# Optimization experiments

Hardware: AMD Instinct MI355X
Metric: run time of the kernel (lower is better)

Reference implementation:

```python
import jax, jax.numpy as jnp
import numpy as np

N, F_IN, HID, C, H = 4096, 1024, 64, 40, 8
ALPHA = 0.2  # LeakyReLU negative slope
NEG_INF = -9e15

def setup_inputs() -> dict:
    key = jax.random.key(0)
    ks = jax.random.split(key, 8)
    x = jax.random.normal(ks[0], (N, F_IN), jnp.float32)
    adj = jax.random.randint(ks[1], (N, N), 0, 2, jnp.int32)  # dense 0/1 adjacency
    W = jax.random.normal(ks[2], (H, F_IN, HID), jnp.float32) / np.sqrt(F_IN).astype(np.float32)
    a_src = jax.random.normal(ks[3], (H, HID), jnp.float32) * 0.1
    a_dst = jax.random.normal(ks[4], (H, HID), jnp.float32) * 0.1
    W_out = jax.random.normal(ks[5], (H * HID, C), jnp.float32) / np.sqrt(H * HID).astype(np.float32)
    ao_src = jax.random.normal(ks[6], (C,), jnp.float32) * 0.1
    ao_dst = jax.random.normal(ks[7], (C,), jnp.float32) * 0.1
    return dict(x=x, adj=adj, W=W, a_src=a_src, a_dst=a_dst,
                W_out=W_out, ao_src=ao_src, ao_dst=ao_dst)

def _masked_attention(src, dst, mask):
    # src: [..., N] scores for row node i; dst: [..., N] scores for col node j
    e = jax.nn.leaky_relu(src[..., :, None] + dst[..., None, :], ALPHA)  # [..., N, N]
    e = jnp.where(mask, e, NEG_INF)
    return jax.nn.softmax(e, axis=-1)

def reference(x, adj, W, a_src, a_dst, W_out, ao_src, ao_dst):
    mask = adj > 0  # [N, N]
    # multi-head GAT layer (concat=True)
    Wh = jnp.einsum('nf,hfo->hno', x, W)            # [H, N, HID]
    src = jnp.einsum('hno,ho->hn', Wh, a_src)       # [H, N]
    dst = jnp.einsum('hno,ho->hn', Wh, a_dst)       # [H, N]
    att = _masked_attention(src, dst, mask[None])   # [H, N, N]
    h = jnp.einsum('hij,hjo->hio', att, Wh)         # [H, N, HID]
    h = jax.nn.elu(h)                               # concat=True -> elu inside layer
    h = jnp.transpose(h, (1, 0, 2)).reshape(N, H * HID)  # concat heads -> [N, H*HID]
    # output GAT layer (concat=False -> no elu inside)
    Wh2 = h @ W_out                                 # [N, C]
    att2 = _masked_attention(Wh2 @ ao_src, Wh2 @ ao_dst, mask)  # [N, N]
    out = att2 @ Wh2                                # [N, C]
    # model-level: elu then log_softmax over classes
    return jax.nn.log_softmax(jax.nn.elu(out), axis=1)
```

## Files before the change

### kernel.cpp

```cpp
#include <hip/hip_runtime.h>

#define NN 4096
#define F_IN 1024
#define NHEAD 8
#define HID 64
#define NCLS 40
#define LOG2E 1.44269504f

typedef float f32x4 __attribute__((ext_vector_type(4)));
typedef float f32x2 __attribute__((ext_vector_type(2)));
typedef short s16x8 __attribute__((ext_vector_type(8)));

#define SWZ(r,c) (((r)*64) + ((c) ^ (((r)&7)<<3)))

__device__ __forceinline__ unsigned short f2bf(float f){
  unsigned u = __float_as_uint(f);
  return (unsigned short)((u + 0x7fffu + ((u >> 16) & 1u)) >> 16);
}
__device__ __forceinline__ unsigned cvtpk(float lo, float hi){
  unsigned r; asm("v_cvt_pk_bf16_f32 %0, %1, %2" : "=v"(r) : "v"(lo), "v"(hi)); return r;
}
__device__ __forceinline__ f32x2 pkmul(f32x2 a, f32x2 b){
  f32x2 r; asm("v_pk_mul_f32 %0, %1, %2" : "=v"(r) : "v"(a), "v"(b)); return r;
}

__global__ __launch_bounds__(256) void pack_adj_k(const int* __restrict__ adj, unsigned* __restrict__ bmT){
  int gid = blockIdx.x*256 + threadIdx.x;
  int lane = threadIdx.x & 63;
  unsigned long long m = __ballot(adj[gid] > 0);
  int w = gid >> 5, i = w >> 7, jw = w & 127;
  if (lane == 0)       bmT[(size_t)jw*NN + i] = (unsigned)m;
  else if (lane == 32) bmT[(size_t)jw*NN + i] = (unsigned)(m >> 32);
}

__global__ __launch_bounds__(256) void cast_W_k(const float* __restrict__ W, unsigned short* __restrict__ WbT){
  __shared__ float T[64][65];
  const int h = blockIdx.y, k0 = blockIdx.x*64, t = threadIdx.x;
  for (int idx = t; idx < 1024; idx += 256){
    int k = idx >> 4, c4 = idx & 15;
    *(float4*)&T[k][c4*4] = *(const float4*)&W[((size_t)h*F_IN + k0 + k)*HID + c4*4];
  }
  __syncthreads();
  for (int idx = t; idx < 512; idx += 256){
    int o = idx >> 3, ch = idx & 7;
    s16x8 v;
    #pragma unroll
    for (int e = 0; e < 8; ++e) v[e] = (short)f2bf(T[ch*8 + e][o]);
    *(s16x8*)&WbT[((size_t)h*HID + o)*F_IN + k0 + ch*8] = v;
  }
}

__global__ __launch_bounds__(256) void cast_Wo_k(const float* __restrict__ Wout, unsigned short* __restrict__ WoT){
  int idx = blockIdx.x*256 + threadIdx.x;
  int cc = idx >> 9, k = idx & 511;
  WoT[idx] = (cc < NCLS) ? f2bf(Wout[(size_t)k*NCLS + cc]) : (unsigned short)0;
}

__global__ __launch_bounds__(256) void gemm1_k(const float* __restrict__ x,
    const unsigned short* __restrict__ WbT, unsigned short* __restrict__ WhT,
    const float* __restrict__ a_src, const float* __restrict__ a_dst,
    float* __restrict__ srcv, float* __restrict__ dstv){
  __shared__ unsigned short xS[64*64];
  __shared__ unsigned short wS[64*64];
  const int t = threadIdx.x, l = t & 63, wv = t >> 6, g = l >> 4, c = l & 15;
  const int h = blockIdx.y, n0 = blockIdx.x * 64;
  f32x4 acc[4] = {};
  for (int k0 = 0; k0 < F_IN; k0 += 64){
    __syncthreads();
    #pragma unroll
    for (int p = 0; p < 4; ++p){
      int idx = t + p*256, row = idx >> 4, c4 = idx & 15;
      float4 v = *(const float4*)&x[(size_t)(n0+row)*F_IN + k0 + c4*4];
      *(uint2*)&xS[SWZ(row, c4*4)] = make_uint2(cvtpk(v.x, v.y), cvtpk(v.z, v.w));
    }
    #pragma unroll
    for (int p = 0; p < 2; ++p){
      int idx = t + p*256, o = idx >> 3, ch = idx & 7;
      *(s16x8*)&wS[SWZ(o, ch*8)] = *(const s16x8*)&WbT[(size_t)(h*HID + o)*F_IN + k0 + ch*8];
    }
    __syncthreads();
    #pragma unroll
    for (int ks = 0; ks < 2; ++ks){
      s16x8 av = *(const s16x8*)&xS[SWZ(wv*16 + c, ks*32 + g*8)];
      #pragma unroll
      for (int ct = 0; ct < 4; ++ct){
        s16x8 bv = *(const s16x8*)&wS[SWZ(ct*16 + c, ks*32 + g*8)];
        acc[ct] = __builtin_amdgcn_mfma_f32_16x16x32_bf16(av, bv, acc[ct], 0, 0, 0);
      }
    }
  }
  float asv[4], adv[4];
  #pragma unroll
  for (int ct = 0; ct < 4; ++ct){ asv[ct] = a_src[h*HID + ct*16 + c]; adv[ct] = a_dst[h*HID + ct*16 + c]; }
  #pragma unroll
  for (int r = 0; r < 4; ++r){
    float ps = acc[0][r]*asv[0] + acc[1][r]*asv[1] + acc[2][r]*asv[2] + acc[3][r]*asv[3];
    float pd = acc[0][r]*adv[0] + acc[1][r]*adv[1] + acc[2][r]*adv[2] + acc[3][r]*adv[3];
    #pragma unroll
    for (int off = 1; off < 16; off <<= 1){ ps += __shfl_xor(ps, off); pd += __shfl_xor(pd, off); }
    if (c == 0){ int n = n0 + wv*16 + g*4 + r; srcv[h*NN + n] = ps; dstv[h*NN + n] = pd; }
  }
  __syncthreads();
  #pragma unroll
  for (int ct = 0; ct < 4; ++ct)
    *(uint2*)&xS[SWZ(ct*16 + c, wv*16 + g*4)] = make_uint2(cvtpk(acc[ct][0], acc[ct][1]), cvtpk(acc[ct][2], acc[ct][3]));
  __syncthreads();
  #pragma unroll
  for (int p = 0; p < 2; ++p){
    int idx = t + p*256, o = idx >> 3, ch = idx & 7;
    *(s16x8*)&WhT[(size_t)(h*HID + o)*NN + n0 + ch*8] = *(const s16x8*)&xS[SWZ(o, ch*8)];
  }
}

__global__ __launch_bounds__(256) void maxred_k(const float* __restrict__ in, float* __restrict__ out){
  __shared__ float red[4];
  const float* p = in + (size_t)blockIdx.x*NN;
  float m = -3.0e38f;
  for (int i = threadIdx.x; i < NN; i += 256) m = fmaxf(m, p[i]);
  #pragma unroll
  for (int off = 32; off; off >>= 1) m = fmaxf(m, __shfl_xor(m, off));
  if ((threadIdx.x & 63) == 0) red[threadIdx.x >> 6] = m;
  __syncthreads();
  if (threadIdx.x == 0) out[blockIdx.x] = fmaxf(fmaxf(red[0], red[1]), fmaxf(red[2], red[3]));
}

template<int NCT, int NJT, bool CHUNKED, bool DO_ELU>
__global__ __launch_bounds__(256) void agg_mfma_k(
    const unsigned* __restrict__ bmT, const unsigned short* __restrict__ VT,
    const float* __restrict__ srcv, const float* __restrict__ dstv,
    const float* __restrict__ maxp, void* __restrict__ outp)
{
  __shared__ unsigned short vS[2][2][NCT*16*64];
  __shared__ float2 dS[2][2][64];
  __shared__ unsigned bitS[2][2][2][32];
  const int t = threadIdx.x, l = t & 63, wv = t >> 6, g = l >> 4, c = l & 15;
  const int h   = CHUNKED ? 0 : blockIdx.y;
  const int jt0 = CHUNKED ? blockIdx.y * NJT : 0;
  const int i0 = blockIdx.x * 32;
  const int tl = wv >> 1, rH = wv & 1;
  const int lr = rH*16 + c;
  const float sr = srcv[h*NN + i0 + lr];
  const float mx = maxp[CHUNKED ? 0 : h];
  const float tm = sr + mx;
  const float mi2 = fmaxf(tm, 0.2f*tm) * LOG2E;
  f32x2 ac2;
  ac2[0] = exp2f(fmaf(sr, LOG2E, -mi2));
  ac2[1] = exp2f(fmaf(0.2f*sr, LOG2E, -mi2));
  const unsigned short* vb = VT + (size_t)h*HID*NN;

  f32x4 acc[NCT] = {};
  f32x4 accs = {};
  s16x8 ones;
  #pragma unroll
  for (int e = 0; e < 8; ++e) ones[e] = (short)0x3F80;

  s16x8 vreg[NCT]; float2 dreg = make_float2(0.f, 0.f); unsigned breg = 0;
  auto loadRegs = [&](int jt){
    #pragma unroll
    for (int p = 0; p < NCT; ++p){
      int u = t + p*256;
      int tt = u / (NCT*128), rem = u % (NCT*128);
      int o = rem >> 3, chk = rem & 7;
      vreg[p] = *(const s16x8*)&vb[(size_t)o*NN + (jt+tt)*64 + chk*8];
    }
    if (t < 128){
      float d = dstv[h*NN + (jt + (t>>6))*64 + (t&63)];
      dreg = make_float2(exp2f(d*LOG2E), exp2f(0.2f*d*LOG2E));
    }
    else { int u = t - 128; breg = bmT[(size_t)((jt + (u>>6))*2 + ((u>>5)&1))*NN + i0 + (u&31)]; }
  };
  auto writeLDS = [&](int b){
    #pragma unroll
    for (int p = 0; p < NCT; ++p){
      int u = t + p*256;
      int tt = u / (NCT*128), rem = u % (NCT*128);
      int o = rem >> 3, chk = rem & 7;
      *(s16x8*)&vS[b][tt][SWZ(o, chk*8)] = vreg[p];
    }
    if (t < 128) dS[b][t>>6][t&63] = dreg;
    else { int u = t - 128; bitS[b][u>>6][(u>>5)&1][u&31] = breg; }
  };
  auto computeBuf = [&](int b){
    #pragma unroll
    for (int ks = 0; ks < 2; ++ks){
      unsigned wb = (bitS[b][tl][ks][lr] >> (g*8)) & 0xffu;
      const f32x2* dr = (const f32x2*)&dS[b][tl][ks*32 + g*8];
      float q[8];
      #pragma unroll
      for (int e = 0; e < 8; ++e){
        f32x2 pr = pkmul(ac2, dr[e]);
        float m3 = __builtin_amdgcn_fmed3f(pr[0], pr[1], 1.0f);
        q[e] = (wb & (1u << e)) ? m3 : 0.f;
      }
      s16x8 af;
      ((unsigned*)&af)[0] = cvtpk(q[0], q[1]);
      ((unsigned*)&af)[1] = cvtpk(q[2], q[3]);
      ((unsigned*)&af)[2] = cvtpk(q[4], q[5]);
      ((unsigned*)&af)[3] = cvtpk(q[6], q[7]);
      #pragma unroll
      for (int ct = 0; ct < NCT; ++ct){
        s16x8 bv = *(const s16x8*)&vS[b][tl][SWZ(ct*16 + c, ks*32 + g*8)];
        acc[ct] = __builtin_amdgcn_mfma_f32_16x16x32_bf16(af, bv, acc[ct], 0, 0, 0);
      }
      accs = __builtin_amdgcn_mfma_f32_16x16x32_bf16(af, ones, accs, 0, 0, 0);
    }
  };

  loadRegs(jt0);
  writeLDS(0);
  __syncthreads();
  int cur = 0;
  for (int jj = 0; jj < NJT; jj += 2){
    const bool more = (jj + 2 < NJT);
    if (more) loadRegs(jt0 + jj + 2);
    computeBuf(cur);
    if (more) writeLDS(cur ^ 1);
    __syncthreads();
    cur ^= 1;
  }

  float* mrg = (float*)&vS[0][0][0];
  constexpr int S = (NCT + 1) * 4;
  if (tl == 1){
    int base = (rH*64 + l) * S;
    #pragma unroll
    for (int ct = 0; ct < NCT; ++ct)
      #pragma unroll
      for (int r = 0; r < 4; ++r) mrg[base + ct*4 + r] = acc[ct][r];
    #pragma unroll
    for (int r = 0; r < 4; ++r) mrg[base + NCT*4 + r] = accs[r];
  }
  __syncthreads();
  if (tl == 0){
    int base = (rH*64 + l) * S;
    #pragma unroll
    for (int ct = 0; ct < NCT; ++ct)
      #pragma unroll
      for (int r = 0; r < 4; ++r) acc[ct][r] += mrg[base + ct*4 + r];
    #pragma unroll
    for (int r = 0; r < 4; ++r) accs[r] += mrg[base + NCT*4 + r];
    if (!CHUNKED){
      unsigned short* ob = (unsigned short*)outp;
      #pragma unroll
      for (int r = 0; r < 4; ++r){
        float inv = 1.f / fmaxf(accs[r], 1e-30f);
        int row = i0 + rH*16 + g*4 + r;
        #pragma unroll
        for (int ct = 0; ct < NCT; ++ct){
          float v = acc[ct][r] * inv;
          if (DO_ELU) v = v > 0.f ? v : __expf(v) - 1.f;
          ob[(size_t)row*(NHEAD*HID) + h*HID + ct*16 + c] = f2bf(v);
        }
      }
    } else {
      float* ob = (float*)outp + (size_t)blockIdx.y * NN * 64;
      #pragma unroll
      for (int r = 0; r < 4; ++r){
        int row = i0 + rH*16 + g*4 + r;
        #pragma unroll
        for (int ct = 0; ct < NCT; ++ct)
          ob[(size_t)row*64 + ct*16 + c] = acc[ct][r];
        if (c == 0) ob[(size_t)row*64 + 48] = accs[r];
      }
    }
  }
}

__global__ __launch_bounds__(256) void gemm2_k(const unsigned short* __restrict__ hb,
    const unsigned short* __restrict__ WoT, const float* __restrict__ aos, const float* __restrict__ aod,
    unsigned short* __restrict__ WhT2, float* __restrict__ s2, float* __restrict__ d2){
  __shared__ unsigned short aS[64*64];
  __shared__ unsigned short bS[48*64];
  const int t = threadIdx.x, l = t & 63, wv = t >> 6, g = l >> 4, c = l & 15;
  const int n0 = blockIdx.x * 64;
  f32x4 acc[3] = {};
  for (int k0 = 0; k0 < NHEAD*HID; k0 += 64){
    __syncthreads();
    #pragma unroll
    for (int p = 0; p < 2; ++p){
      int u = t + p*256, o = u >> 3, ch = u & 7;
      *(s16x8*)&aS[SWZ(o, ch*8)] = *(const s16x8*)&hb[(size_t)(n0+o)*(NHEAD*HID) + k0 + ch*8];
    }
    for (int u = t; u < 384; u += 256){
      int o = u >> 3, ch = u & 7;
      *(s16x8*)&bS[SWZ(o, ch*8)] = *(const s16x8*)&WoT[(size_t)o*(NHEAD*HID) + k0 + ch*8];
    }
    __syncthreads();
    #pragma unroll
    for (int ks = 0; ks < 2; ++ks){
      s16x8 av = *(const s16x8*)&aS[SWZ(wv*16 + c, ks*32 + g*8)];
      #pragma unroll
      for (int ct = 0; ct < 3; ++ct){
        s16x8 bv = *(const s16x8*)&bS[SWZ(ct*16 + c, ks*32 + g*8)];
        acc[ct] = __builtin_amdgcn_mfma_f32_16x16x32_bf16(av, bv, acc[ct], 0, 0, 0);
      }
    }
  }
  float asv[3], adv[3];
  #pragma unroll
  for (int ct = 0; ct < 3; ++ct){
    int col = ct*16 + c;
    asv[ct] = (col < NCLS) ? aos[col] : 0.f;
    adv[ct] = (col < NCLS) ? aod[col] : 0.f;
  }
  #pragma unroll
  for (int r = 0; r < 4; ++r){
    float ps = acc[0][r]*asv[0] + acc[1][r]*asv[1] + acc[2][r]*asv[2];
    float pd = acc[0][r]*adv[0] + acc[1][r]*adv[1] + acc[2][r]*adv[2];
    #pragma unroll
    for (int off = 1; off < 16; off <<= 1){ ps += __shfl_xor(ps, off); pd += __shfl_xor(pd, off); }
    if (c == 0){ int n = n0 + wv*16 + g*4 + r; s2[n] = ps; d2[n] = pd; }
  }
  __syncthreads();
  #pragma unroll
  for (int ct = 0; ct < 3; ++ct)
    *(uint2*)&bS[SWZ(ct*16 + c, wv*16 + g*4)] = make_uint2(cvtpk(acc[ct][0], acc[ct][1]), cvtpk(acc[ct][2], acc[ct][3]));
  __syncthreads();
  for (int u = t; u < 384; u += 256){
    int o = u >> 3, ch = u & 7;
    *(s16x8*)&WhT2[(size_t)o*NN + n0 + ch*8] = *(const s16x8*)&bS[SWZ(o, ch*8)];
  }
}

__global__ __launch_bounds__(256) void final_k(const float* __restrict__ part, float* __restrict__ out){
  const int wid = (blockIdx.x*256 + threadIdx.x) >> 6;
  const int c = threadIdx.x & 63;
  float acc = 0.f, rs = 0.f;
  #pragma unroll
  for (int ch = 0; ch < 8; ++ch){
    const float* pb = part + ((size_t)ch*NN + wid)*64;
    if (c < 48) acc += pb[c];
    rs += pb[48];
  }
  float v = acc / fmaxf(rs, 1e-30f);
  float e = v > 0.f ? v : __expf(v) - 1.f;
  float ev = (c < NCLS) ? e : -3.0e38f;
  float m = ev;
  #pragma unroll
  for (int off = 32; off; off >>= 1) m = fmaxf(m, __shfl_xor(m, off));
  float ex = (c < NCLS) ? __expf(e - m) : 0.f;
  float s = ex;
  #pragma unroll
  for (int off = 32; off; off >>= 1) s += __shfl_xor(s, off);
  if (c < NCLS) out[(size_t)wid*NCLS + c] = e - m - __logf(s);
}

extern "C" void kernel_launch(void* const* d_in, const int* in_sizes, int n_in,
                              void* d_out, int out_size, void* d_ws, size_t ws_size,
                              hipStream_t stream){
  (void)in_sizes; (void)n_in; (void)out_size; (void)ws_size;
  const float* x     = (const float*)d_in[0];
  const int*   adj   = (const int*)  d_in[1];
  const float* W     = (const float*)d_in[2];
  const float* a_src = (const float*)d_in[3];
  const float* a_dst = (const float*)d_in[4];
  const float* W_out = (const float*)d_in[5];
  const float* aos   = (const float*)d_in[6];
  const float* aod   = (const float*)d_in[7];
  float* out = (float*)d_out;

  char* p = (char*)d_ws;
  unsigned* bmT        = (unsigned*)p;       p += (size_t)NN*128*4;
  unsigned short* WbT  = (unsigned short*)p; p += (size_t)NHEAD*HID*F_IN*2;
  unsigned short* WhT  = (unsigned short*)p; p += (size_t)NHEAD*HID*NN*2;
  unsigned short* hbuf = (unsigned short*)p; p += (size_t)NN*NHEAD*HID*2;
  unsigned short* WoT  = (unsigned short*)p; p += (size_t)48*NHEAD*HID*2;
  unsigned short* WhT2 = (unsigned short*)p; p += (size_t)48*NN*2;
  float* srcv = (float*)p; p += (size_t)NHEAD*NN*4;
  float* dstv = (float*)p; p += (size_t)NHEAD*NN*4;
  float* maxd = (float*)p; p += 256;
  float* s2   = (float*)p; p += (size_t)NN*4;
  float* d2   = (float*)p; p += (size_t)NN*4;
  float* m2   = (float*)p; p += 256;
  float* part = (float*)p; p += (size_t)8*NN*64*4;

  pack_adj_k<<<(NN*NN)/256, 256, 0, stream>>>(adj, bmT);
  cast_W_k<<<dim3(F_IN/64, NHEAD), 256, 0, stream>>>(W, WbT);
  cast_Wo_k<<<96, 256, 0, stream>>>(W_out, WoT);
  gemm1_k<<<dim3(NN/64, NHEAD), 256, 0, stream>>>(x, WbT, WhT, a_src, a_dst, srcv, dstv);
  maxred_k<<<NHEAD, 256, 0, stream>>>(dstv, maxd);
  agg_mfma_k<4, 64, false, true><<<dim3(NN/32, NHEAD), 256, 0, stream>>>(bmT, WhT, srcv, dstv, maxd, hbuf);
  gemm2_k<<<NN/64, 256, 0, stream>>>(hbuf, WoT, aos, aod, WhT2, s2, d2);
  maxred_k<<<1, 256, 0, stream>>>(d2, m2);
  agg_mfma_k<3, 8, true, false><<<dim3(NN/32, 8), 256, 0, stream>>>(bmT, WhT2, s2, d2, m2, part);
  final_k<<<NN/4, 256, 0, stream>>>(part, out);
}
```

Before: 157.1 us.

## Precompute exp of dst scores in GEMM epilogues; read bits and dst directly in aggregation

The exp2 terms of the destination scores are now computed once in the gemm1/gemm2 epilogues and stored as float2 arrays, instead of being recomputed per tile in every aggregation block. The aggregation kernel no longer stages adjacency bits and dst exponentials through LDS; each wave loads its bitmask words and dst pairs straight from global/L2 inside computeBuf. The V-tile LDS reads are also hoisted ahead of the weight computation. This saves LDS traffic and redundant exp work, but adds uncached-latency global loads inside the compute loop that are not prefetched.

New measurement: 163.3 us. 4.0% more time.

```diff
diff --git a/kernel.cpp b/kernel.cpp
--- a/kernel.cpp
+++ b/kernel.cpp
@@ -59,7 +59,7 @@
 __global__ __launch_bounds__(256) void gemm1_k(const float* __restrict__ x,
     const unsigned short* __restrict__ WbT, unsigned short* __restrict__ WhT,
     const float* __restrict__ a_src, const float* __restrict__ a_dst,
-    float* __restrict__ srcv, float* __restrict__ dstv){
+    float* __restrict__ srcv, float* __restrict__ dstv, float2* __restrict__ bdv){
   __shared__ unsigned short xS[64*64];
   __shared__ unsigned short wS[64*64];
   const int t = threadIdx.x, l = t & 63, wv = t >> 6, g = l >> 4, c = l & 15;
@@ -98,7 +98,11 @@
     float pd = acc[0][r]*adv[0] + acc[1][r]*adv[1] + acc[2][r]*adv[2] + acc[3][r]*adv[3];
     #pragma unroll
     for (int off = 1; off < 16; off <<= 1){ ps += __shfl_xor(ps, off); pd += __shfl_xor(pd, off); }
-    if (c == 0){ int n = n0 + wv*16 + g*4 + r; srcv[h*NN + n] = ps; dstv[h*NN + n] = pd; }
+    if (c == 0){
+      int n = n0 + wv*16 + g*4 + r;
+      srcv[h*NN + n] = ps; dstv[h*NN + n] = pd;
+      bdv[h*NN + n] = make_float2(exp2f(pd*LOG2E), exp2f(0.2f*pd*LOG2E));
+    }
   }
   __syncthreads();
   #pragma unroll
@@ -127,12 +131,10 @@
 template<int NCT, int NJT, bool CHUNKED, bool DO_ELU>
 __global__ __launch_bounds__(256) void agg_mfma_k(
     const unsigned* __restrict__ bmT, const unsigned short* __restrict__ VT,
-    const float* __restrict__ srcv, const float* __restrict__ dstv,
+    const float* __restrict__ srcv, const float2* __restrict__ bdv,
     const float* __restrict__ maxp, void* __restrict__ outp)
 {
   __shared__ unsigned short vS[2][2][NCT*16*64];
-  __shared__ float2 dS[2][2][64];
-  __shared__ unsigned bitS[2][2][2][32];
   const int t = threadIdx.x, l = t & 63, wv = t >> 6, g = l >> 4, c = l & 15;
   const int h   = CHUNKED ? 0 : blockIdx.y;
   const int jt0 = CHUNKED ? blockIdx.y * NJT : 0;
@@ -146,7 +148,8 @@
   f32x2 ac2;
   ac2[0] = exp2f(fmaf(sr, LOG2E, -mi2));
   ac2[1] = exp2f(fmaf(0.2f*sr, LOG2E, -mi2));
-  const unsigned short* vb = VT + (size_t)h*HID*NN;
+  const unsigned short* vb = VT + (CHUNKED ? (size_t)0 : (size_t)h*HID*NN);
+  const float2* bp = bdv + (CHUNKED ? (size_t)0 : (size_t)h*NN);
 
   f32x4 acc[NCT] = {};
   f32x4 accs = {};
@@ -154,7 +157,7 @@
   #pragma unroll
   for (int e = 0; e < 8; ++e) ones[e] = (short)0x3F80;
 
-  s16x8 vreg[NCT]; float2 dreg = make_float2(0.f, 0.f); unsigned breg = 0;
+  s16x8 vreg[NCT];
   auto loadRegs = [&](int jt){
     #pragma unroll
     for (int p = 0; p < NCT; ++p){
@@ -163,11 +166,6 @@
       int o = rem >> 3, chk = rem & 7;
       vreg[p] = *(const s16x8*)&vb[(size_t)o*NN + (jt+tt)*64 + chk*8];
     }
-    if (t < 128){
-      float d = dstv[h*NN + (jt + (t>>6))*64 + (t&63)];
-      dreg = make_float2(exp2f(d*LOG2E), exp2f(0.2f*d*LOG2E));
-    }
-    else { int u = t - 128; breg = bmT[(size_t)((jt + (u>>6))*2 + ((u>>5)&1))*NN + i0 + (u&31)]; }
   };
   auto writeLDS = [&](int b){
     #pragma unroll
@@ -177,32 +175,37 @@
       int o = rem >> 3, chk = rem & 7;
       *(s16x8*)&vS[b][tt][SWZ(o, chk*8)] = vreg[p];
     }
-    if (t < 128) dS[b][t>>6][t&63] = dreg;
-    else { int u = t - 128; bitS[b][u>>6][(u>>5)&1][u&31] = breg; }
   };
-  auto computeBuf = [&](int b){
+  auto computeBuf = [&](int b, int jtile){
+    unsigned wbit[2];
+    wbit[0] = bmT[(size_t)(jtile*2 + 0)*NN + i0 + lr];
+    wbit[1] = bmT[(size_t)(jtile*2 + 1)*NN + i0 + lr];
     #pragma unroll
     for (int ks = 0; ks < 2; ++ks){
-      unsigned wb = (bitS[b][tl][ks][lr] >> (g*8)) & 0xffu;
-      const f32x2* dr = (const f32x2*)&dS[b][tl][ks*32 + g*8];
+      f32x2 drv[8];
+      #pragma unroll
+      for (int e = 0; e < 8; ++e) drv[e] = *(const f32x2*)&bp[jtile*64 + ks*32 + g*8 + e];
+      s16x8 bv[NCT];
+      #pragma unroll
+      for (int ct = 0; ct < NCT; ++ct)
+        bv[ct] = *(const s16x8*)&vS[b][tl][SWZ(ct*16 + c, ks*32 + g*8)];
+      unsigned wb = (wbit[ks] >> (g*8)) & 0xffu;
       float q[8];
       #pragma unroll
       for (int e = 0; e < 8; ++e){
-        f32x2 pr = pkmul(ac2, dr[e]);
+        f32x2 pr = pkmul(ac2, drv[e]);
         float m3 = __builtin_amdgcn_fmed3f(pr[0], pr[1], 1.0f);
         q[e] = (wb & (1u << e)) ? m3 : 0.f;
       }
-      s16x8 af;
-      ((unsigned*)&af)[0] = cvtpk(q[0], q[1]);
-      ((unsigned*)&af)[1] = cvtpk(q[2], q[3]);
-      ((unsigned*)&af)[2] = cvtpk(q[4], q[5]);
-      ((unsigned*)&af)[3] = cvtpk(q[6], q[7]);
-      #pragma unroll
-      for (int ct = 0; ct < NCT; ++ct){
-        s16x8 bv = *(const s16x8*)&vS[b][tl][SWZ(ct*16 + c, ks*32 + g*8)];
-        acc[ct] = __builtin_amdgcn_mfma_f32_16x16x32_bf16(af, bv, acc[ct], 0, 0, 0);
-      }
-      accs = __builtin_amdgcn_mfma_f32_16x16x32_bf16(af, ones, accs, 0, 0, 0);
+      s16x8 afr;
+      ((unsigned*)&afr)[0] = cvtpk(q[0], q[1]);
+      ((unsigned*)&afr)[1] = cvtpk(q[2], q[3]);
+      ((unsigned*)&afr)[2] = cvtpk(q[4], q[5]);
+      ((unsigned*)&afr)[3] = cvtpk(q[6], q[7]);
+      #pragma unroll
+      for (int ct = 0; ct < NCT; ++ct)
+        acc[ct] = __builtin_amdgcn_mfma_f32_16x16x32_bf16(afr, bv[ct], acc[ct], 0, 0, 0);
+      accs = __builtin_amdgcn_mfma_f32_16x16x32_bf16(afr, ones, accs, 0, 0, 0);
     }
   };
 
@@ -213,7 +216,7 @@
   for (int jj = 0; jj < NJT; jj += 2){
     const bool more = (jj + 2 < NJT);
     if (more) loadRegs(jt0 + jj + 2);
-    computeBuf(cur);
+    computeBuf(cur, jt0 + jj + tl);
     if (more) writeLDS(cur ^ 1);
     __syncthreads();
     cur ^= 1;
@@ -268,7 +271,8 @@
 
 __global__ __launch_bounds__(256) void gemm2_k(const unsigned short* __restrict__ hb,
     const unsigned short* __restrict__ WoT, const float* __restrict__ aos, const float* __restrict__ aod,
-    unsigned short* __restrict__ WhT2, float* __restrict__ s2, float* __restrict__ d2){
+    unsigned short* __restrict__ WhT2, float* __restrict__ s2, float* __restrict__ d2,
+    float2* __restrict__ bd2){
   __shared__ unsigned short aS[64*64];
   __shared__ unsigned short bS[48*64];
   const int t = threadIdx.x, l = t & 63, wv = t >> 6, g = l >> 4, c = l & 15;
@@ -309,7 +313,11 @@
     float pd = acc[0][r]*adv[0] + acc[1][r]*adv[1] + acc[2][r]*adv[2];
     #pragma unroll
     for (int off = 1; off < 16; off <<= 1){ ps += __shfl_xor(ps, off); pd += __shfl_xor(pd, off); }
-    if (c == 0){ int n = n0 + wv*16 + g*4 + r; s2[n] = ps; d2[n] = pd; }
+    if (c == 0){
+      int n = n0 + wv*16 + g*4 + r;
+      s2[n] = ps; d2[n] = pd;
+      bd2[n] = make_float2(exp2f(pd*LOG2E), exp2f(0.2f*pd*LOG2E));
+    }
   }
   __syncthreads();
   #pragma unroll
@@ -372,16 +380,18 @@
   float* s2   = (float*)p; p += (size_t)NN*4;
   float* d2   = (float*)p; p += (size_t)NN*4;
   float* m2   = (float*)p; p += 256;
+  float2* bdv1 = (float2*)p; p += (size_t)NHEAD*NN*8;
+  float2* bdv2 = (float2*)p; p += (size_t)NN*8;
   float* part = (float*)p; p += (size_t)8*NN*64*4;
 
   pack_adj_k<<<(NN*NN)/256, 256, 0, stream>>>(adj, bmT);
   cast_W_k<<<dim3(F_IN/64, NHEAD), 256, 0, stream>>>(W, WbT);
   cast_Wo_k<<<96, 256, 0, stream>>>(W_out, WoT);
-  gemm1_k<<<dim3(NN/64, NHEAD), 256, 0, stream>>>(x, WbT, WhT, a_src, a_dst, srcv, dstv);
+  gemm1_k<<<dim3(NN/64, NHEAD), 256, 0, stream>>>(x, WbT, WhT, a_src, a_dst, srcv, dstv, bdv1);
   maxred_k<<<NHEAD, 256, 0, stream>>>(dstv, maxd);
-  agg_mfma_k<4, 64, false, true><<<dim3(NN/32, NHEAD), 256, 0, stream>>>(bmT, WhT, srcv, dstv, maxd, hbuf);
-  gemm2_k<<<NN/64, 256, 0, stream>>>(hbuf, WoT, aos, aod, WhT2, s2, d2);
+  agg_mfma_k<4, 64, false, true><<<dim3(NN/32, NHEAD), 256, 0, stream>>>(bmT, WhT, srcv, bdv1, maxd, hbuf);
+  gemm2_k<<<NN/64, 256, 0, stream>>>(hbuf, WoT, aos, aod, WhT2, s2, d2, bdv2);
   maxred_k<<<1, 256, 0, stream>>>(d2, m2);
-  agg_mfma_k<3, 8, true, false><<<dim3(NN/32, 8), 256, 0, stream>>>(bmT, WhT2, s2, d2, m2, part);
+  agg_mfma_k<3, 8, true, false><<<dim3(NN/32, 8), 256, 0, stream>>>(bmT, WhT2, s2, bdv2, m2, part);
   final_k<<<NN/4, 256, 0, stream>>>(part, out);
 }
```
